# Kernel tuning notes

Hardware: AMD Instinct MI355X
Metric: run time of the kernel (lower is better)

## Reference

```python
import jax, jax.numpy as jnp
import numpy as np

M = 100_000   # output rows of neighborhood matrix
N = 100_000   # nodes
D = 64        # feature dim (in_channels)
OUT = 64      # out_channels
NNZ = 1_600_000
NEG_SLOPE = 0.2


def setup_inputs() -> dict:
    key = jax.random.key(0)
    k1, k2, k3, k4, k5 = jax.random.split(key, 5)
    # ensure every row has at least one neighbor (torch min init is +inf otherwise)
    rows = jnp.concatenate([jnp.arange(M, dtype=jnp.int32),
                            jax.random.randint(k1, (NNZ - M,), 0, M, dtype=jnp.int32)])
    cols = jax.random.randint(k2, (NNZ,), 0, N, dtype=jnp.int32)
    vals = jnp.ones((NNZ,), jnp.float32)
    node_features = jax.random.normal(k3, (N, D), jnp.float32)
    W = jax.random.normal(k4, (OUT, 12 * D), jnp.float32) / jnp.sqrt(12.0 * D)
    b = jax.random.normal(k5, (OUT,), jnp.float32) * 0.01
    return {"rows": rows, "cols": cols, "vals": vals,
            "node_features": node_features, "W": W, "b": b}


def reference(rows, cols, vals, node_features, W, b):
    gathered = node_features[cols]                      # [nnz, D]
    deg = jax.ops.segment_sum(vals, rows, num_segments=M)[:, None]  # [M,1]
    valid = deg > 0
    safe_deg = jnp.where(valid, deg, 1.0)

    # mean = spmm(A, X) / deg on valid rows (torch leaves invalid rows as raw sum = 0)
    sums = jax.ops.segment_sum(vals[:, None] * gathered, rows, num_segments=M)
    mean = jnp.where(valid, sums / safe_deg, sums)

    # torch max starts from zeros -> clamps at 0 from below; empty rows stay 0
    maxf = jnp.zeros((M, D), node_features.dtype).at[rows].max(gathered)
    # torch min starts from +inf; all rows covered by construction
    minf = jnp.full((M, D), jnp.inf, node_features.dtype).at[rows].min(gathered)

    sq = jax.ops.segment_sum(vals[:, None] * gathered**2, rows, num_segments=M)
    sq = jnp.where(valid, sq / safe_deg, sq)
    std = jnp.sqrt(jnp.clip(sq - mean**2, 0.0))

    logd = jnp.log10(deg + 2.0)                          # [M,1]
    delta = jnp.mean(logd)
    s = logd / delta

    # per aggregator: identity, amplification (*s), attenuation (/s)
    feats = [t for a in (mean, maxf, minf, std) for t in (a, a * s, a / s)]
    X = jnp.concatenate(feats, axis=1)                   # [M, 12*D]
    out = X @ W.T + b
    return jnp.where(out >= 0, out, NEG_SLOPE * out)
```

## Files before the change

### kernel.cpp

```cpp
#include <hip/hip_runtime.h>
#include <cstdint>

#define M_ROWS   100000
#define N_NODES  100000
#define NNZ_E    1600000
#define K_DIM    768
#define NCHUNK   24
#define NEG_SLOPE 0.2f
#define NBUK     391
#define BCAP     5120
#define EPB      8192
#define WB_ELEMS (NCHUNK * 4 * 64 * 8)
#define NFWB_BLOCKS ((N_NODES * 16 + WB_ELEMS + 255) / 256)

using f32x4 = __attribute__((ext_vector_type(4))) float;
using f16x8 = __attribute__((ext_vector_type(8))) _Float16;
using f16x4 = __attribute__((ext_vector_type(4))) _Float16;

#define OFF_CNT    0u
#define OFF_RS     401408u
#define OFF_PART   802816u
#define OFF_DELTA  804864u
#define OFF_GCUR   805120u
#define OFF_BINCSR 807168u
#define OFF_WB     8814848u
#define OFF_NFH    8913152u
#define WS_NEEDED  21713152u

__global__ void k_wb(const float* __restrict__ W, _Float16* __restrict__ Wb) {
  int idx = blockIdx.x * blockDim.x + threadIdx.x;
  if (idx < WB_ELEMS) {
    int i  = idx & 7;
    int l  = (idx >> 3) & 63;
    int n  = (idx >> 9) & 3;
    int kc = idx >> 11;
    int k  = kc * 32 + ((l >> 4) << 3) + i;
    int o  = n * 16 + (l & 15);
    Wb[idx] = (_Float16)W[o * K_DIM + k];
  }
}

__global__ __launch_bounds__(256) void k_nfwb(const float* __restrict__ nf,
                                              _Float16* __restrict__ nfh,
                                              const float* __restrict__ W,
                                              _Float16* __restrict__ Wb,
                                              int* __restrict__ gcur) {
  const int gid = blockIdx.x * 256 + threadIdx.x;
  if (gid < NBUK) gcur[gid] = gid * BCAP;
  if (gid < N_NODES * 16) {
    const int i = gid * 4;
    const f32x4 v = *reinterpret_cast<const f32x4*>(nf + i);
    f16x4 h;
    #pragma unroll
    for (int j = 0; j < 4; ++j) h[j] = (_Float16)v[j];
    *reinterpret_cast<f16x4*>(nfh + i) = h;
  } else {
    const int idx = gid - N_NODES * 16;
    if (idx < WB_ELEMS) {
      const int i  = idx & 7;
      const int l  = (idx >> 3) & 63;
      const int n  = (idx >> 9) & 3;
      const int kc = idx >> 11;
      const int k  = kc * 32 + ((l >> 4) << 3) + i;
      const int o  = n * 16 + (l & 15);
      Wb[idx] = (_Float16)W[o * K_DIM + k];
    }
  }
}

__global__ void k_seed(int* __restrict__ gcur) {
  int b = blockIdx.x * blockDim.x + threadIdx.x;
  if (b < NBUK) gcur[b] = b * BCAP;
}

__global__ __launch_bounds__(256) void k_bin(const int* __restrict__ rows,
                                             const int* __restrict__ cols,
                                             int* __restrict__ gcur,
                                             int* __restrict__ binArr) {
  __shared__ int hist[NBUK];
  __shared__ int base_s[NBUK];
  const int t  = threadIdx.x;
  const int e0 = blockIdx.x * EPB;
  for (int b = t; b < NBUK; b += 256) hist[b] = 0;
  __syncthreads();
  for (int i = 0; i < EPB / 256; ++i) {
    const int e = e0 + i * 256 + t;
    if (e < NNZ_E) atomicAdd(&hist[rows[e] >> 8], 1);
  }
  __syncthreads();
  for (int b = t; b < NBUK; b += 256) {
    const int h = hist[b];
    base_s[b] = h ? atomicAdd(&gcur[b], h) : 0;
    hist[b] = 0;
  }
  __syncthreads();
  for (int i = 0; i < EPB / 256; ++i) {
    const int e = e0 + i * 256 + t;
    if (e < NNZ_E) {
      const int r = rows[e], c = cols[e], b = r >> 8;
      const int p = atomicAdd(&hist[b], 1);
      const int slot = base_s[b] + p;
      if (slot < (b + 1) * BCAP)
        binArr[slot] = ((r & 255) << 24) | c;
    }
  }
}

__global__ __launch_bounds__(256) void k_sortbucket(int* __restrict__ bincsr,
                                                    const int* __restrict__ gcur,
                                                    int* __restrict__ cnt,
                                                    int* __restrict__ row_start,
                                                    float* __restrict__ partial) {
  __shared__ int se[BCAP];
  __shared__ int hist[256];
  __shared__ int curs[256];
  __shared__ int sd[256];
  __shared__ float wsum[4];
  const int b = blockIdx.x, t = threadIdx.x;
  const int s0  = b * BCAP;
  const int len = min(gcur[b] - s0, BCAP);
  for (int i = t; i < len; i += 256) se[i] = bincsr[s0 + i];
  hist[t] = 0;
  __syncthreads();
  for (int i = t; i < len; i += 256)
    atomicAdd(&hist[((unsigned)se[i]) >> 24], 1);
  __syncthreads();
  const int h = hist[t];
  const int r = (b << 8) + t;
  sd[t] = h;
  __syncthreads();
  #pragma unroll
  for (int off = 1; off < 256; off <<= 1) {
    int add = (t >= off) ? sd[t - off] : 0;
    __syncthreads();
    sd[t] += add;
    __syncthreads();
  }
  const int excl = sd[t] - h;
  curs[t] = excl;
  if (r < M_ROWS) {
    cnt[r] = h;
    row_start[r] = s0 + excl;
  }
  float ls = (r < M_ROWS) ? log10f((float)h + 2.0f) : 0.f;
  #pragma unroll
  for (int off = 32; off > 0; off >>= 1) ls += __shfl_xor(ls, off);
  if ((t & 63) == 0) wsum[t >> 6] = ls;
  __syncthreads();
  if (t == 0) partial[b] = wsum[0] + wsum[1] + wsum[2] + wsum[3];
  for (int i = t; i < len; i += 256) {
    const int e  = se[i];
    const int rl = (int)(((unsigned)e) >> 24);
    const int p  = atomicAdd(&curs[rl], 1);
    bincsr[s0 + p] = (e & 0x00FFFFFF) << 7;
  }
}

__global__ void k_delta(const float* __restrict__ partial, float* __restrict__ delta) {
  __shared__ float sd[256];
  const int t = threadIdx.x;
  float s = 0.f;
  for (int i = t; i < NBUK; i += 256) s += partial[i];
  sd[t] = s;
  __syncthreads();
  for (int off = 128; off > 0; off >>= 1) {
    if (t < off) sd[t] += sd[t + off];
    __syncthreads();
  }
  if (t == 0) delta[0] = sd[0] / (float)M_ROWS;
}

template <bool F16NF>
__global__ __launch_bounds__(256) void k_main(
    const float* __restrict__ nf32, const _Float16* __restrict__ nfh,
    const int* __restrict__ csr, const int* __restrict__ rs,
    const int* __restrict__ cnt, const float* __restrict__ delta_p,
    const _Float16* __restrict__ Wb, const float* __restrict__ bias,
    float* __restrict__ out)
{
  __shared__ _Float16 xs[32][264];
  __shared__ float s_s[32];

  const int tid  = threadIdx.x;
  const int w    = tid >> 6;
  const int lane = tid & 63;
  const int g    = lane >> 4;
  const int q    = lane & 15;
  const int h    = (lane >> 3) & 1;
  const int d    = lane & 7;
  const int r0   = blockIdx.x * 32;
  const float delta = delta_p[0];
  const int d16  = d * 16;

  auto ld16 = [&](int off) -> f16x8 {
    if constexpr (F16NF) {
      return *reinterpret_cast<const f16x8*>((const char*)nfh + off + d16);
    } else {
      const char* p = (const char*)nf32 + (size_t)off * 2 + d * 32;
      const f32x4 a = *reinterpret_cast<const f32x4*>(p);
      const f32x4 c = *reinterpret_cast<const f32x4*>(p + 16);
      f16x8 x;
      #pragma unroll
      for (int j = 0; j < 4; ++j) { x[j] = (_Float16)a[j]; x[4 + j] = (_Float16)c[j]; }
      return x;
    }
  };

  auto xor8 = [&](f16x8 v) -> f16x8 {
    union { f16x8 hh; int ii[4]; } u;
    u.hh = v;
    #pragma unroll
    for (int k = 0; k < 4; ++k) u.ii[k] = __shfl_xor(u.ii[k], 8);
    return u.hh;
  };

  #pragma unroll
  for (int pass = 0; pass < 2; ++pass) {
    const int rl  = w * 8 + pass * 4 + g;
    const int r   = r0 + rl;
    const int js  = rs[r];
    const int len = cnt[r];
    const int full8 = len & ~7;
    const int tailn = len - full8;
    int mfull = full8, mtail = tailn;
    mfull = max(mfull, __shfl_xor(mfull, 16));
    mfull = max(mfull, __shfl_xor(mfull, 32));
    mtail = max(mtail, __shfl_xor(mtail, 16));
    mtail = max(mtail, __shfl_xor(mtail, 32));

    f16x8 hsum = {}; f16x8 hsq = {}; f16x8 hmx = {};
    f16x8 hmn = {(_Float16)INFINITY, (_Float16)INFINITY, (_Float16)INFINITY,
                 (_Float16)INFINITY, (_Float16)INFINITY, (_Float16)INFINITY,
                 (_Float16)INFINITY, (_Float16)INFINITY};

    const int jb = js + h;

    for (int t = 0; t < mfull; t += 8) {
      if (t < full8) {
        const int i0 = csr[jb + t + 0];
        const int i1 = csr[jb + t + 2];
        const int i2 = csr[jb + t + 4];
        const int i3 = csr[jb + t + 6];
        const f16x8 x0 = ld16(i0), x1 = ld16(i1), x2 = ld16(i2), x3 = ld16(i3);
        hmx = __builtin_elementwise_max(hmx, x0);
        hmn = __builtin_elementwise_min(hmn, x0);
        hsum += x0; hsq += x0 * x0;
        hmx = __builtin_elementwise_max(hmx, x1);
        hmn = __builtin_elementwise_min(hmn, x1);
        hsum += x1; hsq += x1 * x1;
        hmx = __builtin_elementwise_max(hmx, x2);
        hmn = __builtin_elementwise_min(hmn, x2);
        hsum += x2; hsq += x2 * x2;
        hmx = __builtin_elementwise_max(hmx, x3);
        hmn = __builtin_elementwise_min(hmn, x3);
        hsum += x3; hsq += x3 * x3;
      }
    }

    if (mtail > 0) {
      const int last = js + len - 1;
      const int e0 = full8 + 0 + h, e1 = full8 + 2 + h;
      const int e2 = full8 + 4 + h, e3 = full8 + 6 + h;
      const int i0 = csr[min(jb + full8 + 0, last)];
      const int i1 = csr[min(jb + full8 + 2, last)];
      const int i2 = csr[min(jb + full8 + 4, last)];
      const int i3 = csr[min(jb + full8 + 6, last)];
      const f16x8 x0 = ld16(i0), x1 = ld16(i1), x2 = ld16(i2), x3 = ld16(i3);
      const f16x8 z = {};
      const f16x8 m0 = (e0 < len) ? x0 : z;
      const f16x8 m1 = (e1 < len) ? x1 : z;
      const f16x8 m2 = (e2 < len) ? x2 : z;
      const f16x8 m3 = (e3 < len) ? x3 : z;
      hmx = __builtin_elementwise_max(hmx, x0);
      hmn = __builtin_elementwise_min(hmn, x0);
      hsum += m0; hsq += m0 * x0;
      hmx = __builtin_elementwise_max(hmx, x1);
      hmn = __builtin_elementwise_min(hmn, x1);
      hsum += m1; hsq += m1 * x1;
      hmx = __builtin_elementwise_max(hmx, x2);
      hmn = __builtin_elementwise_min(hmn, x2);
      hsum += m2; hsq += m2 * x2;
      hmx = __builtin_elementwise_max(hmx, x3);
      hmn = __builtin_elementwise_min(hmn, x3);
      hsum += m3; hsq += m3 * x3;
    }

    hsum += xor8(hsum);
    hsq  += xor8(hsq);
    hmx = __builtin_elementwise_max(hmx, xor8(hmx));
    hmn = __builtin_elementwise_min(hmn, xor8(hmn));

    const float dg  = (float)len;
    const float inv = 1.0f / fmaxf(dg, 1.0f);
    f16x8 hmean, hstd;
    #pragma unroll
    for (int i = 0; i < 8; ++i) {
      const float mean = (float)hsum[i] * inv;
      const float sqm  = (float)hsq[i] * inv;
      const float var  = fmaxf(sqm - mean * mean, 0.f);
      hmean[i] = (_Float16)mean;
      hstd[i]  = (_Float16)sqrtf(var);
    }
    if (h == 0) {
      *reinterpret_cast<f16x8*>(&xs[rl][0 * 64 + d * 8]) = hmean;
      *reinterpret_cast<f16x8*>(&xs[rl][1 * 64 + d * 8]) = hmx;
      *reinterpret_cast<f16x8*>(&xs[rl][2 * 64 + d * 8]) = hmn;
      *reinterpret_cast<f16x8*>(&xs[rl][3 * 64 + d * 8]) = hstd;
      if (q == 0) s_s[rl] = log10f(dg + 2.0f) / delta;
    }
  }
  __syncthreads();

  f32x4 acc0 = {0.f, 0.f, 0.f, 0.f}, acc1 = {0.f, 0.f, 0.f, 0.f};
  const int khi = lane >> 4;
  const float sA = s_s[q];
  const float sB = s_s[16 + q];
  const f16x8 sA8  = (f16x8)(_Float16)sA;
  const f16x8 isA8 = (f16x8)(_Float16)(1.0f / sA);
  const f16x8 sB8  = (f16x8)(_Float16)sB;
  const f16x8 isB8 = (f16x8)(_Float16)(1.0f / sB);

  #pragma unroll
  for (int kc = 0; kc < NCHUNK; ++kc) {
    const int kb = kc >> 1;
    const int a  = kb / 3;
    const int tt = kb - 3 * a;
    const int off = a * 64 + ((kc & 1) << 5) + (khi << 3);
    f16x8 a0 = *reinterpret_cast<const f16x8*>(&xs[q][off]);
    f16x8 a1 = *reinterpret_cast<const f16x8*>(&xs[16 + q][off]);
    if (tt == 1) { a0 = a0 * sA8;  a1 = a1 * sB8; }
    if (tt == 2) { a0 = a0 * isA8; a1 = a1 * isB8; }
    const f16x8 bf = *reinterpret_cast<const f16x8*>(Wb + ((size_t)(kc * 4 + w) * 64 + lane) * 8);
    acc0 = __builtin_amdgcn_mfma_f32_16x16x32_f16(a0, bf, acc0, 0, 0, 0);
    acc1 = __builtin_amdgcn_mfma_f32_16x16x32_f16(a1, bf, acc1, 0, 0, 0);
  }

  const int col = w * 16 + q;
  const float bv = bias[col];
  #pragma unroll
  for (int i = 0; i < 4; ++i) {
    const int rr = khi * 4 + i;
    float v = acc0[i] + bv;
    v = (v >= 0.f) ? v : NEG_SLOPE * v;
    out[(size_t)(r0 + rr) * 64 + col] = v;
    float u = acc1[i] + bv;
    u = (u >= 0.f) ? u : NEG_SLOPE * u;
    out[(size_t)(r0 + 16 + rr) * 64 + col] = u;
  }
}

extern "C" void kernel_launch(void* const* d_in, const int* in_sizes, int n_in,
                              void* d_out, int out_size, void* d_ws, size_t ws_size,
                              hipStream_t stream) {
  const int*   rows = (const int*)d_in[0];
  const int*   cols = (const int*)d_in[1];
  const float* nf   = (const float*)d_in[3];
  const float* W    = (const float*)d_in[4];
  const float* bias = (const float*)d_in[5];
  float* out = (float*)d_out;

  char* ws = (char*)d_ws;
  int*      cnt       = (int*)(ws + OFF_CNT);
  int*      row_start = (int*)(ws + OFF_RS);
  float*    partial   = (float*)(ws + OFF_PART);
  float*    delta     = (float*)(ws + OFF_DELTA);
  int*      gcur      = (int*)(ws + OFF_GCUR);
  int*      bincsr    = (int*)(ws + OFF_BINCSR);
  _Float16* Wb        = (_Float16*)(ws + OFF_WB);
  _Float16* nfh       = (_Float16*)(ws + OFF_NFH);

  const bool f16path = (ws_size >= WS_NEEDED);

  if (f16path) {
    k_nfwb<<<NFWB_BLOCKS, 256, 0, stream>>>(nf, nfh, W, Wb, gcur);
  } else {
    k_wb<<<192, 256, 0, stream>>>(W, Wb);
    k_seed<<<2, 256, 0, stream>>>(gcur);
  }
  k_bin<<<(NNZ_E + EPB - 1) / EPB, 256, 0, stream>>>(rows, cols, gcur, bincsr);
  k_sortbucket<<<NBUK, 256, 0, stream>>>(bincsr, gcur, cnt, row_start, partial);
  k_delta<<<1, 256, 0, stream>>>(partial, delta);
  if (f16path)
    k_main<true><<<M_ROWS / 32, 256, 0, stream>>>(nf, nfh, bincsr, row_start, cnt, delta, Wb, bias, out);
  else
    k_main<false><<<M_ROWS / 32, 256, 0, stream>>>(nf, nfh, bincsr, row_start, cnt, delta, Wb, bias, out);
}
```

Baseline: 105.0 us.

## Fuse binning with conversion kernel and fold delta reduction into main kernel

Merges the edge-binning kernel with the feature/weight fp16 conversion kernel into one launch that uses distinct block ranges, and replaces the gcur seeding with a memset of relative counters. It drops the single-block delta kernel by having every main-kernel block reduce the 391 partial sums itself. It also vectorizes the rows/cols loads in binning to int4. This removes two kernel launches and their serialization gaps, at the cost of redundant partial-sum reduction and extra syncs in every main block.

```diff
diff --git a/kernel.cpp b/kernel.cpp
--- a/kernel.cpp
+++ b/kernel.cpp
@@ -10,8 +10,9 @@
 #define NBUK     391
 #define BCAP     5120
 #define EPB      8192
+#define BIN_BLOCKS ((NNZ_E + EPB - 1) / EPB)
 #define WB_ELEMS (NCHUNK * 4 * 64 * 8)
-#define NFWB_BLOCKS ((N_NODES * 16 + WB_ELEMS + 255) / 256)
+#define NF_THREADS (N_NODES * 16)
 
 using f32x4 = __attribute__((ext_vector_type(4))) float;
 using f16x8 = __attribute__((ext_vector_type(8))) _Float16;
@@ -20,42 +21,77 @@
 #define OFF_CNT    0u
 #define OFF_RS     401408u
 #define OFF_PART   802816u
-#define OFF_DELTA  804864u
 #define OFF_GCUR   805120u
 #define OFF_BINCSR 807168u
 #define OFF_WB     8814848u
 #define OFF_NFH    8913152u
 #define WS_NEEDED  21713152u
 
-__global__ void k_wb(const float* __restrict__ W, _Float16* __restrict__ Wb) {
-  int idx = blockIdx.x * blockDim.x + threadIdx.x;
-  if (idx < WB_ELEMS) {
-    int i  = idx & 7;
-    int l  = (idx >> 3) & 63;
-    int n  = (idx >> 9) & 3;
-    int kc = idx >> 11;
-    int k  = kc * 32 + ((l >> 4) << 3) + i;
-    int o  = n * 16 + (l & 15);
-    Wb[idx] = (_Float16)W[o * K_DIM + k];
-  }
-}
-
-__global__ __launch_bounds__(256) void k_nfwb(const float* __restrict__ nf,
-                                              _Float16* __restrict__ nfh,
-                                              const float* __restrict__ W,
-                                              _Float16* __restrict__ Wb,
-                                              int* __restrict__ gcur) {
-  const int gid = blockIdx.x * 256 + threadIdx.x;
-  if (gid < NBUK) gcur[gid] = gid * BCAP;
-  if (gid < N_NODES * 16) {
-    const int i = gid * 4;
-    const f32x4 v = *reinterpret_cast<const f32x4*>(nf + i);
-    f16x4 h;
+template <bool DO_NF>
+__global__ __launch_bounds__(256) void k_prep2(const int* __restrict__ rows,
+                                               const int* __restrict__ cols,
+                                               int* __restrict__ gcur,
+                                               int* __restrict__ binArr,
+                                               const float* __restrict__ nf,
+                                               _Float16* __restrict__ nfh,
+                                               const float* __restrict__ W,
+                                               _Float16* __restrict__ Wb) {
+  __shared__ int hist[NBUK];
+  __shared__ int base_s[NBUK];
+  const int t = threadIdx.x;
+
+  if (blockIdx.x < BIN_BLOCKS) {
+    const int e0 = blockIdx.x * EPB;
+    for (int b = t; b < NBUK; b += 256) hist[b] = 0;
+    __syncthreads();
     #pragma unroll
-    for (int j = 0; j < 4; ++j) h[j] = (_Float16)v[j];
-    *reinterpret_cast<f16x4*>(nfh + i) = h;
+    for (int i = 0; i < EPB / 1024; ++i) {
+      const int e = e0 + i * 1024 + t * 4;
+      if (e < NNZ_E) {
+        const int4 r4 = *reinterpret_cast<const int4*>(rows + e);
+        atomicAdd(&hist[r4.x >> 8], 1); atomicAdd(&hist[r4.y >> 8], 1);
+        atomicAdd(&hist[r4.z >> 8], 1); atomicAdd(&hist[r4.w >> 8], 1);
+      }
+    }
+    __syncthreads();
+    for (int b = t; b < NBUK; b += 256) {
+      const int h = hist[b];
+      base_s[b] = (h ? atomicAdd(&gcur[b], h) : 0) + b * BCAP;
+      hist[b] = 0;
+    }
+    __syncthreads();
+    #pragma unroll
+    for (int i = 0; i < EPB / 1024; ++i) {
+      const int e = e0 + i * 1024 + t * 4;
+      if (e < NNZ_E) {
+        const int4 r4 = *reinterpret_cast<const int4*>(rows + e);
+        const int4 c4 = *reinterpret_cast<const int4*>(cols + e);
+        #pragma unroll
+        for (int k = 0; k < 4; ++k) {
+          const int r = (k == 0) ? r4.x : (k == 1) ? r4.y : (k == 2) ? r4.z : r4.w;
+          const int c = (k == 0) ? c4.x : (k == 1) ? c4.y : (k == 2) ? c4.z : c4.w;
+          const int b = r >> 8;
+          const int p = atomicAdd(&hist[b], 1);
+          const int slot = base_s[b] + p;
+          if (slot < (b + 1) * BCAP)
+            binArr[slot] = ((r & 255) << 24) | c;
+        }
+      }
+    }
   } else {
-    const int idx = gid - N_NODES * 16;
+    const int gid = (blockIdx.x - BIN_BLOCKS) * 256 + t;
+    if (DO_NF) {
+      if (gid < NF_THREADS) {
+        const int i = gid * 4;
+        const f32x4 v = *reinterpret_cast<const f32x4*>(nf + i);
+        f16x4 h;
+        #pragma unroll
+        for (int j = 0; j < 4; ++j) h[j] = (_Float16)v[j];
+        *reinterpret_cast<f16x4*>(nfh + i) = h;
+        return;
+      }
+    }
+    const int idx = DO_NF ? (gid - NF_THREADS) : gid;
     if (idx < WB_ELEMS) {
       const int i  = idx & 7;
       const int l  = (idx >> 3) & 63;
@@ -64,44 +100,6 @@
       const int k  = kc * 32 + ((l >> 4) << 3) + i;
       const int o  = n * 16 + (l & 15);
       Wb[idx] = (_Float16)W[o * K_DIM + k];
-    }
-  }
-}
-
-__global__ void k_seed(int* __restrict__ gcur) {
-  int b = blockIdx.x * blockDim.x + threadIdx.x;
-  if (b < NBUK) gcur[b] = b * BCAP;
-}
-
-__global__ __launch_bounds__(256) void k_bin(const int* __restrict__ rows,
-                                             const int* __restrict__ cols,
-                                             int* __restrict__ gcur,
-                                             int* __restrict__ binArr) {
-  __shared__ int hist[NBUK];
-  __shared__ int base_s[NBUK];
-  const int t  = threadIdx.x;
-  const int e0 = blockIdx.x * EPB;
-  for (int b = t; b < NBUK; b += 256) hist[b] = 0;
-  __syncthreads();
-  for (int i = 0; i < EPB / 256; ++i) {
-    const int e = e0 + i * 256 + t;
-    if (e < NNZ_E) atomicAdd(&hist[rows[e] >> 8], 1);
-  }
-  __syncthreads();
-  for (int b = t; b < NBUK; b += 256) {
-    const int h = hist[b];
-    base_s[b] = h ? atomicAdd(&gcur[b], h) : 0;
-    hist[b] = 0;
-  }
-  __syncthreads();
-  for (int i = 0; i < EPB / 256; ++i) {
-    const int e = e0 + i * 256 + t;
-    if (e < NNZ_E) {
-      const int r = rows[e], c = cols[e], b = r >> 8;
-      const int p = atomicAdd(&hist[b], 1);
-      const int slot = base_s[b] + p;
-      if (slot < (b + 1) * BCAP)
-        binArr[slot] = ((r & 255) << 24) | c;
     }
   }
 }
@@ -118,7 +116,7 @@
   __shared__ float wsum[4];
   const int b = blockIdx.x, t = threadIdx.x;
   const int s0  = b * BCAP;
-  const int len = min(gcur[b] - s0, BCAP);
+  const int len = min(gcur[b], BCAP);
   for (int i = t; i < len; i += 256) se[i] = bincsr[s0 + i];
   hist[t] = 0;
   __syncthreads();
@@ -156,30 +154,17 @@
   }
 }
 
-__global__ void k_delta(const float* __restrict__ partial, float* __restrict__ delta) {
-  __shared__ float sd[256];
-  const int t = threadIdx.x;
-  float s = 0.f;
-  for (int i = t; i < NBUK; i += 256) s += partial[i];
-  sd[t] = s;
-  __syncthreads();
-  for (int off = 128; off > 0; off >>= 1) {
-    if (t < off) sd[t] += sd[t + off];
-    __syncthreads();
-  }
-  if (t == 0) delta[0] = sd[0] / (float)M_ROWS;
-}
-
 template <bool F16NF>
 __global__ __launch_bounds__(256) void k_main(
     const float* __restrict__ nf32, const _Float16* __restrict__ nfh,
     const int* __restrict__ csr, const int* __restrict__ rs,
-    const int* __restrict__ cnt, const float* __restrict__ delta_p,
+    const int* __restrict__ cnt, const float* __restrict__ partial,
     const _Float16* __restrict__ Wb, const float* __restrict__ bias,
     float* __restrict__ out)
 {
   __shared__ _Float16 xs[32][264];
   __shared__ float s_s[32];
+  __shared__ float red[256];
 
   const int tid  = threadIdx.x;
   const int w    = tid >> 6;
@@ -189,8 +174,18 @@
   const int h    = (lane >> 3) & 1;
   const int d    = lane & 7;
   const int r0   = blockIdx.x * 32;
-  const float delta = delta_p[0];
   const int d16  = d * 16;
+
+  float ps = 0.f;
+  for (int i = tid; i < NBUK; i += 256) ps += partial[i];
+  red[tid] = ps;
+  __syncthreads();
+  #pragma unroll
+  for (int off = 128; off > 0; off >>= 1) {
+    if (tid < off) red[tid] += red[tid + off];
+    __syncthreads();
+  }
+  const float delta = red[0] / (float)M_ROWS;
 
   auto ld16 = [&](int off) -> f16x8 {
     if constexpr (F16NF) {
@@ -363,7 +358,6 @@
   int*      cnt       = (int*)(ws + OFF_CNT);
   int*      row_start = (int*)(ws + OFF_RS);
   float*    partial   = (float*)(ws + OFF_PART);
-  float*    delta     = (float*)(ws + OFF_DELTA);
   int*      gcur      = (int*)(ws + OFF_GCUR);
   int*      bincsr    = (int*)(ws + OFF_BINCSR);
   _Float16* Wb        = (_Float16*)(ws + OFF_WB);
@@ -371,17 +365,22 @@
 
   const bool f16path = (ws_size >= WS_NEEDED);
 
+  hipMemsetAsync(gcur, 0, NBUK * 4, stream);
+
   if (f16path) {
-    k_nfwb<<<NFWB_BLOCKS, 256, 0, stream>>>(nf, nfh, W, Wb, gcur);
+    const int tail = (NF_THREADS + WB_ELEMS + 255) / 256;
+    k_prep2<true><<<BIN_BLOCKS + tail, 256, 0, stream>>>(rows, cols, gcur, bincsr,
+                                                         nf, nfh, W, Wb);
   } else {
-    k_wb<<<192, 256, 0, stream>>>(W, Wb);
-    k_seed<<<2, 256, 0, stream>>>(gcur);
-  }
-  k_bin<<<(NNZ_E + EPB - 1) / EPB, 256, 0, stream>>>(rows, cols, gcur, bincsr);
+    const int tail = (WB_ELEMS + 255) / 256;
+    k_prep2<false><<<BIN_BLOCKS + tail, 256, 0, stream>>>(rows, cols, gcur, bincsr,
+                                                          nf, nfh, W, Wb);
+  }
   k_sortbucket<<<NBUK, 256, 0, stream>>>(bincsr, gcur, cnt, row_start, partial);
-  k_delta<<<1, 256, 0, stream>>>(partial, delta);
   if (f16path)
-    k_main<true><<<M_ROWS / 32, 256, 0, stream>>>(nf, nfh, bincsr, row_start, cnt, delta, Wb, bias, out);
+    k_main<true><<<M_ROWS / 32, 256, 0, stream>>>(nf, nfh, bincsr, row_start, cnt,
+                                                  partial, Wb, bias, out);
   else
-    k_main<false><<<M_ROWS / 32, 256, 0, stream>>>(nf, nfh, bincsr, row_start, cnt, delta, Wb, bias, out);
+    k_main<false><<<M_ROWS / 32, 256, 0, stream>>>(nf, nfh, bincsr, row_start, cnt,
+                                                   partial, Wb, bias, out);
 }
```

Measured after the change: 93.72 us. -10.7%, faster.
